# Performance work log

Hardware: AMD Instinct MI355X
Metric: run time of the kernel (lower is better)

Reference implementation:

```python
import jax, jax.numpy as jnp
import numpy as np

N, R, H, OUT = 512, 16, 16, 1
EPSILON = 1e-6
CUTOFF = 5.0  # ExpNormalSmearing cutoff_upper (cutoff_lower = 0)


def exp_normal_smearing(dist):
    # dist: (N, N, 1) -> (N, N, R); TorchMD-Net style ExpNormalSmearing
    start = jnp.exp(-CUTOFF)
    means = jnp.linspace(start, 1.0, R, dtype=dist.dtype)
    beta = (2.0 / R * (1.0 - start)) ** -2
    cutoff = 0.5 * (jnp.cos(dist * jnp.pi / CUTOFF) + 1.0) * (dist < CUTOFF)
    return cutoff * jnp.exp(-beta * (jnp.exp(-dist) - means) ** 2)


def setup_inputs() -> dict:
    key = jax.random.key(0)
    ks = jax.random.split(key, 9)
    s_in = 1.0 / np.sqrt(H * H)
    s_h = 1.0 / np.sqrt(H)
    return {
        "x": jax.random.normal(ks[0], (N, 3), jnp.float32) * 1.5,
        "W": jax.random.normal(ks[1], (2, N, R, H), jnp.float32) * 0.1,
        "W1": jax.random.normal(ks[2], (H, H * H), jnp.float32) * s_in,
        "b1": jax.random.normal(ks[3], (H,), jnp.float32) * 0.01,
        "W2": jax.random.normal(ks[4], (4 * R * H, H), jnp.float32) * s_h,
        "W3": jax.random.normal(ks[5], (H, H * H), jnp.float32) * s_in,
        "b3": jax.random.normal(ks[6], (H,), jnp.float32) * 0.01,
        "W4": jax.random.normal(ks[7], (OUT, H), jnp.float32) * s_h,
        "b4": jax.random.normal(ks[8], (OUT,), jnp.float32) * 0.01,
    }


def reference(x, W, W1, b1, W2, W3, b3, W4, b4):
    K, Q = W[0], W[1]                               # (N, R, H) each
    diff = x[:, None, :] - x[None, :, :]            # (N, N, 3)
    nsq = jnp.sum(diff * diff, axis=-1, keepdims=True) + EPSILON
    norm = jnp.sqrt(nsq)                            # (N, N, 1)
    diff = diff / nsq                               # note: divided by squared norm (faithful)
    sm = exp_normal_smearing(norm)                  # (N, N, R)
    basis = sm[..., None] * diff[..., None, :]      # (N, N, R, 3)

    bk = jnp.einsum('ijrb,jrc->icb', basis, K)      # (N, H, 3)
    bq = jnp.einsum('ijrb,jrc->icb', basis, Q)
    att = jnp.einsum('ihb,igb->ihg', bk, bq).reshape(N, H * H)
    att = jax.nn.silu(att @ W1.T + b1) @ W2.T       # (N, 4*R*H), second Linear bias-free

    left, right = att[:, : 2 * R * H], att[:, 2 * R * H:]
    pair = left[:, None, :] + right[None, :, :]     # (N, N, 2*R*H)
    K2 = pair[..., : R * H].reshape(N, N, R, H)
    Q2 = pair[..., R * H:].reshape(N, N, R, H)

    bk = jnp.einsum('ijrb,ijrc->icb', basis, K2)    # (N, H, 3)
    bq = jnp.einsum('ijrb,ijrc->icb', basis, Q2)
    att = jnp.einsum('ihb,igb->ihg', bk, bq).reshape(N, H * H)
    return jax.nn.silu(att @ W3.T + b3) @ W4.T + b4  # (N, OUT)
```

## Files before the change

kernel.cpp:

```cpp
#include <hip/hip_runtime.h>
#include <math.h>

#define NN 512

#define START 0.006737946999085467f
#define STEP  ((1.0f - START) * (1.0f/15.0f))
#define SB    (0.125f * (1.0f - START))
#define BETA  (1.0f/(SB*SB))
#define LOG2E 1.4426950408889634f
#define NB    (-(BETA)*LOG2E)


__global__ __launch_bounds__(256) void k0(const float* __restrict__ W,
                                          float* __restrict__ Wt)
{
    __shared__ float ldsb[256];
    const int row = blockIdx.x;
    ldsb[threadIdx.x] = W[(size_t)row*256 + threadIdx.x];
    __syncthreads();
    const int c = threadIdx.x >> 4, r = threadIdx.x & 15;
    Wt[(size_t)row*256 + threadIdx.x] = ldsb[r*16 + c];
}

__device__ __forceinline__ void dot16(
    float4 g0, float4 g1, float4 g2, float4 g3,
    float4 ka, float4 kb, float4 kc, float4 kd,
    float4 qa, float4 qb, float4 qc, float4 qd,
    float& tk, float& tq)
{
    tk = g0.x*ka.x; tq = g0.x*qa.x;
    tk = fmaf(g0.y,ka.y,tk); tq = fmaf(g0.y,qa.y,tq);
    tk = fmaf(g0.z,ka.z,tk); tq = fmaf(g0.z,qa.z,tq);
    tk = fmaf(g0.w,ka.w,tk); tq = fmaf(g0.w,qa.w,tq);
    tk = fmaf(g1.x,kb.x,tk); tq = fmaf(g1.x,qb.x,tq);
    tk = fmaf(g1.y,kb.y,tk); tq = fmaf(g1.y,qb.y,tq);
    tk = fmaf(g1.z,kb.z,tk); tq = fmaf(g1.z,qb.z,tq);
    tk = fmaf(g1.w,kb.w,tk); tq = fmaf(g1.w,qb.w,tq);
    tk = fmaf(g2.x,kc.x,tk); tq = fmaf(g2.x,qc.x,tq);
    tk = fmaf(g2.y,kc.y,tk); tq = fmaf(g2.y,qc.y,tq);
    tk = fmaf(g2.z,kc.z,tk); tq = fmaf(g2.z,qc.z,tq);
    tk = fmaf(g2.w,kc.w,tk); tq = fmaf(g2.w,qc.w,tq);
    tk = fmaf(g3.x,kd.x,tk); tq = fmaf(g3.x,qd.x,tq);
    tk = fmaf(g3.y,kd.y,tk); tq = fmaf(g3.y,qd.y,tq);
    tk = fmaf(g3.z,kd.z,tk); tq = fmaf(g3.z,qd.z,tq);
    tk = fmaf(g3.w,kd.w,tk); tq = fmaf(g3.w,qd.w,tq);
}

__global__ __launch_bounds__(256) void k1a(const float* __restrict__ x,
                                           const float* __restrict__ Wt,
                                           float* __restrict__ part1)
{
    const int ib = blockIdx.x & 127, jc = blockIdx.x >> 7;
    const int i0 = ib * 4;
    const int tid = threadIdx.x;
    const int c = tid & 15, js = tid >> 4;
    const int lane = tid & 63, wv = tid >> 6;

    __shared__ float  lG[4][64][16];
    __shared__ float4 lP[4][64];
    __shared__ float  s_part[4][16][26];

    {
        const int pi = tid >> 6, pj = tid & 63;
        const int jg = jc*64 + pj;
        const float xi0 = x[(i0+pi)*3+0], xi1 = x[(i0+pi)*3+1], xi2 = x[(i0+pi)*3+2];
        float d0 = xi0 - x[jg*3+0];
        float d1 = xi1 - x[jg*3+1];
        float d2 = xi2 - x[jg*3+2];
        float nsq = fmaf(d0,d0, fmaf(d1,d1, fmaf(d2,d2, 1e-6f)));
        float rs  = __builtin_amdgcn_rsqf(nsq);
        float nrm = nsq * rs;
        float inv = rs * rs;
        float cutv = 0.f;
        if (nrm < 5.0f) cutv = 0.5f*(__cosf(nrm*0.6283185307179586f)+1.0f);
        float en = exp2f(-LOG2E * nrm);
        lP[pi][pj] = make_float4(d0*inv, d1*inv, d2*inv, 0.f);
        float4* dst = reinterpret_cast<float4*>(&lG[pi][pj][0]);
        #pragma unroll
        for (int rq = 0; rq < 4; ++rq) {
            float t0 = en - (START + STEP*(float)(4*rq+0));
            float t1 = en - (START + STEP*(float)(4*rq+1));
            float t2 = en - (START + STEP*(float)(4*rq+2));
            float t3 = en - (START + STEP*(float)(4*rq+3));
            dst[rq] = make_float4(cutv*exp2f(NB*t0*t0), cutv*exp2f(NB*t1*t1),
                                  cutv*exp2f(NB*t2*t2), cutv*exp2f(NB*t3*t3));
        }
    }
    __syncthreads();

    float acc[24];
    #pragma unroll
    for (int v = 0; v < 24; ++v) acc[v] = 0.f;

    const float4* Kp = reinterpret_cast<const float4*>(Wt + (size_t)(jc*64 + js)*256 + c*16);
    const float4* Qp = reinterpret_cast<const float4*>(Wt + (size_t)NN*256 + (size_t)(jc*64 + js)*256 + c*16);
    float4 ka = Kp[0], kb = Kp[1], kc = Kp[2], kd = Kp[3];
    float4 qa = Qp[0], qb = Qp[1], qc = Qp[2], qd = Qp[3];

    #pragma unroll 1
    for (int t = 0; t < 4; ++t) {
        float4 nka, nkb, nkc, nkd, nqa, nqb, nqc, nqd;
        if (t < 3) {
            const float4* Kn = Kp + (size_t)(t+1)*16*64;
            const float4* Qn = Qp + (size_t)(t+1)*16*64;
            nka = Kn[0]; nkb = Kn[1]; nkc = Kn[2]; nkd = Kn[3];
            nqa = Qn[0]; nqb = Qn[1]; nqc = Qn[2]; nqd = Qn[3];
        }
        const int jl = js + 16*t;

        #pragma unroll
        for (int i = 0; i < 4; ++i) {
            const float4* gp = reinterpret_cast<const float4*>(&lG[i][jl][0]);
            float tk, tq;
            dot16(gp[0], gp[1], gp[2], gp[3], ka,kb,kc,kd, qa,qb,qc,qd, tk, tq);
            float4 dd = lP[i][jl];
            acc[i*6+0] = fmaf(tk, dd.x, acc[i*6+0]);
            acc[i*6+1] = fmaf(tk, dd.y, acc[i*6+1]);
            acc[i*6+2] = fmaf(tk, dd.z, acc[i*6+2]);
            acc[i*6+3] = fmaf(tq, dd.x, acc[i*6+3]);
            acc[i*6+4] = fmaf(tq, dd.y, acc[i*6+4]);
            acc[i*6+5] = fmaf(tq, dd.z, acc[i*6+5]);
        }
        if (t < 3) { ka=nka; kb=nkb; kc=nkc; kd=nkd; qa=nqa; qb=nqb; qc=nqc; qd=nqd; }
    }

    #pragma unroll
    for (int v = 0; v < 24; ++v) {
        float t = acc[v];
        t += __shfl_xor(t, 16);
        t += __shfl_xor(t, 32);
        if (lane < 16) s_part[wv][c][v] = t;
    }
    __syncthreads();

    for (int v = tid; v < 384; v += 256) {
        int i = v / 96, o = v - i*96;
        int kq = o / 48, rem = o - kq*48;
        int b = rem >> 4, c2 = rem & 15;
        int f = i*6 + kq*3 + b;
        float sum = s_part[0][c2][f] + s_part[1][c2][f]
                  + s_part[2][c2][f] + s_part[3][c2][f];
        part1[(i0+i)*768 + jc*96 + o] = sum;
    }
}

__global__ __launch_bounds__(256) void k1b(const float* __restrict__ part1,
                                           const float* __restrict__ W1,
                                           const float* __restrict__ b1,
                                           const float* __restrict__ W2,
                                           float* __restrict__ att2t)
{
    const int i = blockIdx.x;
    const int tid = threadIdx.x;
    __shared__ float s_bkq[96];
    __shared__ float s_att[256];
    __shared__ float s_z[16][16];
    __shared__ float s_a1[16];

    if (tid < 96) {
        const float* p = part1 + i*768 + tid;
        float s = 0.f;
        #pragma unroll
        for (int k = 0; k < 8; ++k) s += p[k*96];
        s_bkq[tid] = s;
    }
    __syncthreads();

    {
        int h = tid >> 4, g = tid & 15;
        s_att[tid] = s_bkq[     h]*s_bkq[48+     g]
                   + s_bkq[16 + h]*s_bkq[48+16 + g]
                   + s_bkq[32 + h]*s_bkq[48+32 + g];
    }
    __syncthreads();

    {
        int h = tid & 15, seg = tid >> 4;
        const float* w1 = W1 + h*256 + seg*16;
        const float* a  = s_att + seg*16;
        float p = 0.f;
        #pragma unroll
        for (int k = 0; k < 16; ++k) p = fmaf(a[k], w1[k], p);
        s_z[seg][h] = p;
    }
    __syncthreads();

    if (tid < 16) {
        float z = b1[tid];
        #pragma unroll
        for (int seg = 0; seg < 16; ++seg) z += s_z[seg][tid];
        s_a1[tid] = z / (1.0f + __expf(-z));
    }
    __syncthreads();

    float a1[16];
    #pragma unroll
    for (int cc = 0; cc < 16; ++cc) a1[cc] = s_a1[cc];
    #pragma unroll
    for (int p = 0; p < 4; ++p) {
        int o = tid + p*256;
        const float4* w2 = reinterpret_cast<const float4*>(W2 + o*16);
        float4 wa = w2[0], wb = w2[1], wc = w2[2], wd = w2[3];
        float accv = wa.x*a1[0] + wa.y*a1[1] + wa.z*a1[2] + wa.w*a1[3]
                   + wb.x*a1[4] + wb.y*a1[5] + wb.z*a1[6] + wb.w*a1[7]
                   + wc.x*a1[8] + wc.y*a1[9] + wc.z*a1[10]+ wc.w*a1[11]
                   + wd.x*a1[12]+ wd.y*a1[13]+ wd.z*a1[14]+ wd.w*a1[15];
        att2t[i*1024 + ((o>>8)*256) + ((o&15)*16) + ((o>>4)&15)] = accv;
    }
}

__global__ __launch_bounds__(256) void k2a(const float* __restrict__ x,
                                           const float* __restrict__ att2t,
                                           float* __restrict__ part2)
{
    const int ib = blockIdx.x & 127, jc = blockIdx.x >> 7;
    const int i0 = ib * 4;
    const int tid = threadIdx.x;
    const int c = tid & 15, js = tid >> 4;
    const int lane = tid & 63, wv = tid >> 6;

    __shared__ float  lG[4][64][16];
    __shared__ float4 lP[4][64];
    __shared__ float  s_part[4][16][38];

    {
        const int pi = tid >> 6, pj = tid & 63;
        const int jg = jc*64 + pj;
        const float xi0 = x[(i0+pi)*3+0], xi1 = x[(i0+pi)*3+1], xi2 = x[(i0+pi)*3+2];
        float d0 = xi0 - x[jg*3+0];
        float d1 = xi1 - x[jg*3+1];
        float d2 = xi2 - x[jg*3+2];
        float nsq = fmaf(d0,d0, fmaf(d1,d1, fmaf(d2,d2, 1e-6f)));
        float rs  = __builtin_amdgcn_rsqf(nsq);
        float nrm = nsq * rs;
        float inv = rs * rs;
        float cutv = 0.f;
        if (nrm < 5.0f) cutv = 0.5f*(__cosf(nrm*0.6283185307179586f)+1.0f);
        float en = exp2f(-LOG2E * nrm);
        lP[pi][pj] = make_float4(d0*inv, d1*inv, d2*inv, 0.f);
        float4* dst = reinterpret_cast<float4*>(&lG[pi][pj][0]);
        #pragma unroll
        for (int rq = 0; rq < 4; ++rq) {
            float t0 = en - (START + STEP*(float)(4*rq+0));
            float t1 = en - (START + STEP*(float)(4*rq+1));
            float t2 = en - (START + STEP*(float)(4*rq+2));
            float t3 = en - (START + STEP*(float)(4*rq+3));
            dst[rq] = make_float4(cutv*exp2f(NB*t0*t0), cutv*exp2f(NB*t1*t1),
                                  cutv*exp2f(NB*t2*t2), cutv*exp2f(NB*t3*t3));
        }
    }
    __syncthreads();

    float acc[36];
    #pragma unroll
    for (int v = 0; v < 36; ++v) acc[v] = 0.f;

    const float4* Kp = reinterpret_cast<const float4*>(att2t + (size_t)(jc*64 + js)*1024 + 512 + c*16);
    const float4* Qp = reinterpret_cast<const float4*>(att2t + (size_t)(jc*64 + js)*1024 + 768 + c*16);
    float4 ka = Kp[0], kb = Kp[1], kc = Kp[2], kd = Kp[3];
    float4 qa = Qp[0], qb = Qp[1], qc = Qp[2], qd = Qp[3];

    #pragma unroll 1
    for (int t = 0; t < 4; ++t) {
        float4 nka, nkb, nkc, nkd, nqa, nqb, nqc, nqd;
        if (t < 3) {
            const float4* Kn = Kp + (size_t)(t+1)*16*256;
            const float4* Qn = Qp + (size_t)(t+1)*16*256;
            nka = Kn[0]; nkb = Kn[1]; nkc = Kn[2]; nkd = Kn[3];
            nqa = Qn[0]; nqb = Qn[1]; nqc = Qn[2]; nqd = Qn[3];
        }
        const int jl = js + 16*t;

        #pragma unroll
        for (int i = 0; i < 4; ++i) {
            const float4* gp = reinterpret_cast<const float4*>(&lG[i][jl][0]);
            float tk, tq;
            dot16(gp[0], gp[1], gp[2], gp[3], ka,kb,kc,kd, qa,qb,qc,qd, tk, tq);
            float4 dd = lP[i][jl];
            acc[i*6+0] = fmaf(tk, dd.x, acc[i*6+0]);
            acc[i*6+1] = fmaf(tk, dd.y, acc[i*6+1]);
            acc[i*6+2] = fmaf(tk, dd.z, acc[i*6+2]);
            acc[i*6+3] = fmaf(tq, dd.x, acc[i*6+3]);
            acc[i*6+4] = fmaf(tq, dd.y, acc[i*6+4]);
            acc[i*6+5] = fmaf(tq, dd.z, acc[i*6+5]);
            float gc = lG[i][jl][c];
            acc[24+i*3+0] = fmaf(gc, dd.x, acc[24+i*3+0]);
            acc[24+i*3+1] = fmaf(gc, dd.y, acc[24+i*3+1]);
            acc[24+i*3+2] = fmaf(gc, dd.z, acc[24+i*3+2]);
        }
        if (t < 3) { ka=nka; kb=nkb; kc=nkc; kd=nkd; qa=nqa; qb=nqb; qc=nqc; qd=nqd; }
    }

    #pragma unroll
    for (int v = 0; v < 36; ++v) {
        float t = acc[v];
        t += __shfl_xor(t, 16);
        t += __shfl_xor(t, 32);
        if (lane < 16) s_part[wv][c][v] = t;
    }
    __syncthreads();

    for (int v = tid; v < 576; v += 256) {
        int i = v / 144, o = v - i*144;
        int c2, f;
        if (o < 96) {
            int kq = o / 48, rem = o - kq*48;
            int b = rem >> 4; c2 = rem & 15;
            f = i*6 + kq*3 + b;
        } else {
            int oS = o - 96;
            int r = oS / 3, b = oS - r*3;
            c2 = r;
            f = 24 + i*3 + b;
        }
        float sum = s_part[0][c2][f] + s_part[1][c2][f]
                  + s_part[2][c2][f] + s_part[3][c2][f];
        part2[(i0+i)*1152 + jc*144 + o] = sum;
    }
}

__global__ __launch_bounds__(256) void k2b(const float* __restrict__ att2t,
                                           const float* __restrict__ part2,
                                           const float* __restrict__ W3,
                                           const float* __restrict__ b3,
                                           const float* __restrict__ W4,
                                           const float* __restrict__ b4,
                                           float* __restrict__ out)
{
    const int i = blockIdx.x;
    const int tid = threadIdx.x;
    __shared__ float s_red[144];
    __shared__ float s_att[256];
    __shared__ float s_z[16][16];
    __shared__ float s_a1[16];

    if (tid < 144) {
        const float* p = part2 + i*1152 + tid;
        float s = 0.f;
        #pragma unroll
        for (int k = 0; k < 8; ++k) s += p[k*144];
        s_red[tid] = s;
    }
    __syncthreads();

    if (tid < 96) {
        int kq = tid / 48, rem = tid - kq*48;
        int b = rem >> 4, cc = rem & 15;
        const float4* lrow = reinterpret_cast<const float4*>(att2t + i*1024 + kq*256 + cc*16);
        float4 A = lrow[0], B = lrow[1], C = lrow[2], D = lrow[3];
        float add = 0.f;
        add = fmaf(A.x, s_red[96+ 0*3+b], add);
        add = fmaf(A.y, s_red[96+ 1*3+b], add);
        add = fmaf(A.z, s_red[96+ 2*3+b], add);
        add = fmaf(A.w, s_red[96+ 3*3+b], add);
        add = fmaf(B.x, s_red[96+ 4*3+b], add);
        add = fmaf(B.y, s_red[96+ 5*3+b], add);
        add = fmaf(B.z, s_red[96+ 6*3+b], add);
        add = fmaf(B.w, s_red[96+ 7*3+b], add);
        add = fmaf(C.x, s_red[96+ 8*3+b], add);
        add = fmaf(C.y, s_red[96+ 9*3+b], add);
        add = fmaf(C.z, s_red[96+10*3+b], add);
        add = fmaf(C.w, s_red[96+11*3+b], add);
        add = fmaf(D.x, s_red[96+12*3+b], add);
        add = fmaf(D.y, s_red[96+13*3+b], add);
        add = fmaf(D.z, s_red[96+14*3+b], add);
        add = fmaf(D.w, s_red[96+15*3+b], add);
        s_red[tid] += add;
    }
    __syncthreads();

    {
        int h = tid >> 4, g = tid & 15;
        s_att[tid] = s_red[     h]*s_red[48+     g]
                   + s_red[16 + h]*s_red[48+16 + g]
                   + s_red[32 + h]*s_red[48+32 + g];
    }
    __syncthreads();

    {
        int h = tid & 15, seg = tid >> 4;
        const float* w3 = W3 + h*256 + seg*16;
        const float* a  = s_att + seg*16;
        float p = 0.f;
        #pragma unroll
        for (int k = 0; k < 16; ++k) p = fmaf(a[k], w3[k], p);
        s_z[seg][h] = p;
    }
    __syncthreads();

    if (tid < 16) {
        float z = b3[tid];
        #pragma unroll
        for (int seg = 0; seg < 16; ++seg) z += s_z[seg][tid];
        s_a1[tid] = z / (1.0f + __expf(-z));
    }
    __syncthreads();

    if (tid == 0) {
        float accv = b4[0];
        #pragma unroll
        for (int cc = 0; cc < 16; ++cc) accv = fmaf(s_a1[cc], W4[cc], accv);
        out[i] = accv;
    }
}

extern "C" void kernel_launch(void* const* d_in, const int* in_sizes, int n_in,
                              void* d_out, int out_size, void* d_ws, size_t ws_size,
                              hipStream_t stream) {
    (void)in_sizes; (void)n_in; (void)out_size; (void)ws_size;
    const float* x  = (const float*)d_in[0];
    const float* W  = (const float*)d_in[1];
    const float* W1 = (const float*)d_in[2];
    const float* b1 = (const float*)d_in[3];
    const float* W2 = (const float*)d_in[4];
    const float* W3 = (const float*)d_in[5];
    const float* b3 = (const float*)d_in[6];
    const float* W4 = (const float*)d_in[7];
    const float* b4 = (const float*)d_in[8];

    float* att2t = (float*)d_ws;
    float* part1 = att2t + 512*1024;
    float* part2 = part1 + 512*768;
    float* Wt    = part2 + 512*1152;
    float* out   = (float*)d_out;

    k0 <<<1024, 256, 0, stream>>>(W, Wt);
    k1a<<<1024, 256, 0, stream>>>(x, Wt, part1);
    k1b<<< 512, 256, 0, stream>>>(part1, W1, b1, W2, att2t);
    k2a<<<1024, 256, 0, stream>>>(x, att2t, part2);
    k2b<<< 512, 256, 0, stream>>>(att2t, part2, W3, b3, W4, b4, out);
}
```

Before: 120.9 us.

## Fuse reduction/MLP stages into partial kernels via last-block atomic tickets

Merges k1b into k1a and k2b into k2a. Each block publishes its partial sums with relaxed atomic stores and bumps a per-row-group ticket, and the eighth block to arrive does the cross-chunk reduction and the MLP epilogue for its 4 rows. This removes two kernel launches and their inter-kernel gaps, and tickets are reset in k0. It also drops the register double-buffered prefetch of K/Q in the j-loop, which could expose load latency. The ordering relies only on relaxed atomics with no explicit fences, which carries a memory-visibility risk.

```diff
diff --git a/kernel.cpp b/kernel.cpp
--- a/kernel.cpp
+++ b/kernel.cpp
@@ -11,12 +11,17 @@
 #define NB    (-(BETA)*LOG2E)
 
 
+#define ATOMIC_ST(p, v) __hip_atomic_store((p), (v), __ATOMIC_RELAXED, __HIP_MEMORY_SCOPE_AGENT)
+#define ATOMIC_LD(p)    __hip_atomic_load((p), __ATOMIC_RELAXED, __HIP_MEMORY_SCOPE_AGENT)
+
 __global__ __launch_bounds__(256) void k0(const float* __restrict__ W,
-                                          float* __restrict__ Wt)
+                                          float* __restrict__ Wt,
+                                          unsigned* __restrict__ tick)
 {
     __shared__ float ldsb[256];
     const int row = blockIdx.x;
     ldsb[threadIdx.x] = W[(size_t)row*256 + threadIdx.x];
+    if (blockIdx.x == 0) tick[threadIdx.x] = 0;
     __syncthreads();
     const int c = threadIdx.x >> 4, r = threadIdx.x & 15;
     Wt[(size_t)row*256 + threadIdx.x] = ldsb[r*16 + c];
@@ -46,9 +51,14 @@
     tk = fmaf(g3.w,kd.w,tk); tq = fmaf(g3.w,qd.w,tq);
 }
 
-__global__ __launch_bounds__(256) void k1a(const float* __restrict__ x,
-                                           const float* __restrict__ Wt,
-                                           float* __restrict__ part1)
+__global__ __launch_bounds__(256) void k1(const float* __restrict__ x,
+                                          const float* __restrict__ Wt,
+                                          float* __restrict__ part1,
+                                          const float* __restrict__ W1,
+                                          const float* __restrict__ b1,
+                                          const float* __restrict__ W2,
+                                          float* __restrict__ att2t,
+                                          unsigned* __restrict__ tick)
 {
     const int ib = blockIdx.x & 127, jc = blockIdx.x >> 7;
     const int i0 = ib * 4;
@@ -56,9 +66,15 @@
     const int c = tid & 15, js = tid >> 4;
     const int lane = tid & 63, wv = tid >> 6;
 
-    __shared__ float  lG[4][64][16];
+    __shared__ __align__(16) float  lG[4][64][16];
     __shared__ float4 lP[4][64];
-    __shared__ float  s_part[4][16][26];
+    __shared__ __align__(16) char u_sc[8192];
+    float (*s_part)[16][26] = reinterpret_cast<float(*)[16][26]>(u_sc);
+    float (*s_attf)[256]    = reinterpret_cast<float(*)[256]>(u_sc);
+    float (*s_zf)[16][16]   = reinterpret_cast<float(*)[16][16]>(u_sc + 4096);
+    __shared__ float s_bkq[4][96];
+    __shared__ float s_a1[4][16];
+    __shared__ int   s_flag;
 
     {
         const int pi = tid >> 6, pj = tid & 63;
@@ -92,21 +108,14 @@
     #pragma unroll
     for (int v = 0; v < 24; ++v) acc[v] = 0.f;
 
-    const float4* Kp = reinterpret_cast<const float4*>(Wt + (size_t)(jc*64 + js)*256 + c*16);
-    const float4* Qp = reinterpret_cast<const float4*>(Wt + (size_t)NN*256 + (size_t)(jc*64 + js)*256 + c*16);
-    float4 ka = Kp[0], kb = Kp[1], kc = Kp[2], kd = Kp[3];
-    float4 qa = Qp[0], qb = Qp[1], qc = Qp[2], qd = Qp[3];
-
     #pragma unroll 1
     for (int t = 0; t < 4; ++t) {
-        float4 nka, nkb, nkc, nkd, nqa, nqb, nqc, nqd;
-        if (t < 3) {
-            const float4* Kn = Kp + (size_t)(t+1)*16*64;
-            const float4* Qn = Qp + (size_t)(t+1)*16*64;
-            nka = Kn[0]; nkb = Kn[1]; nkc = Kn[2]; nkd = Kn[3];
-            nqa = Qn[0]; nqb = Qn[1]; nqc = Qn[2]; nqd = Qn[3];
-        }
         const int jl = js + 16*t;
+        const int jg = jc*64 + jl;
+        const float4* Kp = reinterpret_cast<const float4*>(Wt + (size_t)jg*256 + c*16);
+        const float4* Qp = reinterpret_cast<const float4*>(Wt + (size_t)NN*256 + (size_t)jg*256 + c*16);
+        float4 ka = Kp[0], kb = Kp[1], kc = Kp[2], kd = Kp[3];
+        float4 qa = Qp[0], qb = Qp[1], qc = Qp[2], qd = Qp[3];
 
         #pragma unroll
         for (int i = 0; i < 4; ++i) {
@@ -121,7 +130,6 @@
             acc[i*6+4] = fmaf(tq, dd.y, acc[i*6+4]);
             acc[i*6+5] = fmaf(tq, dd.z, acc[i*6+5]);
         }
-        if (t < 3) { ka=nka; kb=nkb; kc=nkc; kd=nkd; qa=nqa; qb=nqb; qc=nqc; qd=nqd; }
     }
 
     #pragma unroll
@@ -140,78 +148,88 @@
         int f = i*6 + kq*3 + b;
         float sum = s_part[0][c2][f] + s_part[1][c2][f]
                   + s_part[2][c2][f] + s_part[3][c2][f];
-        part1[(i0+i)*768 + jc*96 + o] = sum;
-    }
-}
-
-__global__ __launch_bounds__(256) void k1b(const float* __restrict__ part1,
-                                           const float* __restrict__ W1,
-                                           const float* __restrict__ b1,
-                                           const float* __restrict__ W2,
-                                           float* __restrict__ att2t)
-{
-    const int i = blockIdx.x;
-    const int tid = threadIdx.x;
-    __shared__ float s_bkq[96];
-    __shared__ float s_att[256];
-    __shared__ float s_z[16][16];
-    __shared__ float s_a1[16];
-
-    if (tid < 96) {
-        const float* p = part1 + i*768 + tid;
+        ATOMIC_ST(&part1[(i0+i)*768 + jc*96 + o], sum);
+    }
+    __syncthreads();
+
+    if (tid == 0) {
+        unsigned old = __hip_atomic_fetch_add(&tick[ib], 1u,
+                        __ATOMIC_RELAXED, __HIP_MEMORY_SCOPE_AGENT);
+        s_flag = (old == 7u);
+    }
+    __syncthreads();
+    if (!s_flag) return;
+
+    for (int v = tid; v < 384; v += 256) {
+        int ii = v / 96, o = v - ii*96;
+        const float* p = part1 + (i0+ii)*768 + o;
         float s = 0.f;
         #pragma unroll
-        for (int k = 0; k < 8; ++k) s += p[k*96];
-        s_bkq[tid] = s;
-    }
-    __syncthreads();
-
-    {
-        int h = tid >> 4, g = tid & 15;
-        s_att[tid] = s_bkq[     h]*s_bkq[48+     g]
-                   + s_bkq[16 + h]*s_bkq[48+16 + g]
-                   + s_bkq[32 + h]*s_bkq[48+32 + g];
+        for (int k = 0; k < 8; ++k) s += ATOMIC_LD(p + k*96);
+        s_bkq[ii][o] = s;
+    }
+    __syncthreads();
+
+    for (int v = tid; v < 1024; v += 256) {
+        int ii = v >> 8, t2 = v & 255;
+        int h = t2 >> 4, g = t2 & 15;
+        s_attf[ii][t2] = s_bkq[ii][     h]*s_bkq[ii][48+     g]
+                       + s_bkq[ii][16 + h]*s_bkq[ii][48+16 + g]
+                       + s_bkq[ii][32 + h]*s_bkq[ii][48+32 + g];
     }
     __syncthreads();
 
     {
         int h = tid & 15, seg = tid >> 4;
         const float* w1 = W1 + h*256 + seg*16;
-        const float* a  = s_att + seg*16;
-        float p = 0.f;
-        #pragma unroll
-        for (int k = 0; k < 16; ++k) p = fmaf(a[k], w1[k], p);
-        s_z[seg][h] = p;
-    }
-    __syncthreads();
-
-    if (tid < 16) {
-        float z = b1[tid];
-        #pragma unroll
-        for (int seg = 0; seg < 16; ++seg) z += s_z[seg][tid];
-        s_a1[tid] = z / (1.0f + __expf(-z));
-    }
-    __syncthreads();
-
-    float a1[16];
-    #pragma unroll
-    for (int cc = 0; cc < 16; ++cc) a1[cc] = s_a1[cc];
-    #pragma unroll
-    for (int p = 0; p < 4; ++p) {
-        int o = tid + p*256;
-        const float4* w2 = reinterpret_cast<const float4*>(W2 + o*16);
-        float4 wa = w2[0], wb = w2[1], wc = w2[2], wd = w2[3];
-        float accv = wa.x*a1[0] + wa.y*a1[1] + wa.z*a1[2] + wa.w*a1[3]
-                   + wb.x*a1[4] + wb.y*a1[5] + wb.z*a1[6] + wb.w*a1[7]
-                   + wc.x*a1[8] + wc.y*a1[9] + wc.z*a1[10]+ wc.w*a1[11]
-                   + wd.x*a1[12]+ wd.y*a1[13]+ wd.z*a1[14]+ wd.w*a1[15];
-        att2t[i*1024 + ((o>>8)*256) + ((o&15)*16) + ((o>>4)&15)] = accv;
+        #pragma unroll
+        for (int ii = 0; ii < 4; ++ii) {
+            const float* a = &s_attf[ii][seg*16];
+            float p = 0.f;
+            #pragma unroll
+            for (int k = 0; k < 16; ++k) p = fmaf(a[k], w1[k], p);
+            s_zf[ii][seg][h] = p;
+        }
+    }
+    __syncthreads();
+
+    if (tid < 64) {
+        int ii = tid >> 4, h = tid & 15;
+        float z = b1[h];
+        #pragma unroll
+        for (int seg = 0; seg < 16; ++seg) z += s_zf[ii][seg][h];
+        s_a1[ii][h] = z / (1.0f + __expf(-z));
+    }
+    __syncthreads();
+
+    #pragma unroll 1
+    for (int ii = 0; ii < 4; ++ii) {
+        float a1[16];
+        #pragma unroll
+        for (int cc = 0; cc < 16; ++cc) a1[cc] = s_a1[ii][cc];
+        #pragma unroll
+        for (int p = 0; p < 4; ++p) {
+            int o = tid + p*256;
+            const float4* w2 = reinterpret_cast<const float4*>(W2 + o*16);
+            float4 wa = w2[0], wb = w2[1], wc = w2[2], wd = w2[3];
+            float accv = wa.x*a1[0] + wa.y*a1[1] + wa.z*a1[2] + wa.w*a1[3]
+                       + wb.x*a1[4] + wb.y*a1[5] + wb.z*a1[6] + wb.w*a1[7]
+                       + wc.x*a1[8] + wc.y*a1[9] + wc.z*a1[10]+ wc.w*a1[11]
+                       + wd.x*a1[12]+ wd.y*a1[13]+ wd.z*a1[14]+ wd.w*a1[15];
+            att2t[(i0+ii)*1024 + ((o>>8)*256) + ((o&15)*16) + ((o>>4)&15)] = accv;
+        }
     }
 }
 
-__global__ __launch_bounds__(256) void k2a(const float* __restrict__ x,
-                                           const float* __restrict__ att2t,
-                                           float* __restrict__ part2)
+__global__ __launch_bounds__(256) void k2(const float* __restrict__ x,
+                                          const float* __restrict__ att2t,
+                                          float* __restrict__ part2,
+                                          const float* __restrict__ W3,
+                                          const float* __restrict__ b3,
+                                          const float* __restrict__ W4,
+                                          const float* __restrict__ b4,
+                                          float* __restrict__ out,
+                                          unsigned* __restrict__ tick)
 {
     const int ib = blockIdx.x & 127, jc = blockIdx.x >> 7;
     const int i0 = ib * 4;
@@ -219,9 +237,15 @@
     const int c = tid & 15, js = tid >> 4;
     const int lane = tid & 63, wv = tid >> 6;
 
-    __shared__ float  lG[4][64][16];
+    __shared__ __align__(16) float  lG[4][64][16];
     __shared__ float4 lP[4][64];
-    __shared__ float  s_part[4][16][38];
+    __shared__ __align__(16) char u_sc[9728];
+    float (*s_part)[16][38] = reinterpret_cast<float(*)[16][38]>(u_sc);
+    float (*s_attf)[256]    = reinterpret_cast<float(*)[256]>(u_sc);
+    float (*s_zf)[16][16]   = reinterpret_cast<float(*)[16][16]>(u_sc + 4096);
+    __shared__ float s_red[4][144];
+    __shared__ float s_a1[4][16];
+    __shared__ int   s_flag;
 
     {
         const int pi = tid >> 6, pj = tid & 63;
@@ -255,21 +279,14 @@
     #pragma unroll
     for (int v = 0; v < 36; ++v) acc[v] = 0.f;
 
-    const float4* Kp = reinterpret_cast<const float4*>(att2t + (size_t)(jc*64 + js)*1024 + 512 + c*16);
-    const float4* Qp = reinterpret_cast<const float4*>(att2t + (size_t)(jc*64 + js)*1024 + 768 + c*16);
-    float4 ka = Kp[0], kb = Kp[1], kc = Kp[2], kd = Kp[3];
-    float4 qa = Qp[0], qb = Qp[1], qc = Qp[2], qd = Qp[3];
-
     #pragma unroll 1
     for (int t = 0; t < 4; ++t) {
-        float4 nka, nkb, nkc, nkd, nqa, nqb, nqc, nqd;
-        if (t < 3) {
-            const float4* Kn = Kp + (size_t)(t+1)*16*256;
-            const float4* Qn = Qp + (size_t)(t+1)*16*256;
-            nka = Kn[0]; nkb = Kn[1]; nkc = Kn[2]; nkd = Kn[3];
-            nqa = Qn[0]; nqb = Qn[1]; nqc = Qn[2]; nqd = Qn[3];
-        }
         const int jl = js + 16*t;
+        const int jg = jc*64 + jl;
+        const float4* Kp = reinterpret_cast<const float4*>(att2t + (size_t)jg*1024 + 512 + c*16);
+        const float4* Qp = reinterpret_cast<const float4*>(att2t + (size_t)jg*1024 + 768 + c*16);
+        float4 ka = Kp[0], kb = Kp[1], kc = Kp[2], kd = Kp[3];
+        float4 qa = Qp[0], qb = Qp[1], qc = Qp[2], qd = Qp[3];
 
         #pragma unroll
         for (int i = 0; i < 4; ++i) {
@@ -288,7 +305,6 @@
             acc[24+i*3+1] = fmaf(gc, dd.y, acc[24+i*3+1]);
             acc[24+i*3+2] = fmaf(gc, dd.z, acc[24+i*3+2]);
         }
-        if (t < 3) { ka=nka; kb=nkb; kc=nkc; kd=nkd; qa=nqa; qb=nqb; qc=nqc; qd=nqd; }
     }
 
     #pragma unroll
@@ -315,92 +331,93 @@
         }
         float sum = s_part[0][c2][f] + s_part[1][c2][f]
                   + s_part[2][c2][f] + s_part[3][c2][f];
-        part2[(i0+i)*1152 + jc*144 + o] = sum;
-    }
-}
-
-__global__ __launch_bounds__(256) void k2b(const float* __restrict__ att2t,
-                                           const float* __restrict__ part2,
-                                           const float* __restrict__ W3,
-                                           const float* __restrict__ b3,
-                                           const float* __restrict__ W4,
-                                           const float* __restrict__ b4,
-                                           float* __restrict__ out)
-{
-    const int i = blockIdx.x;
-    const int tid = threadIdx.x;
-    __shared__ float s_red[144];
-    __shared__ float s_att[256];
-    __shared__ float s_z[16][16];
-    __shared__ float s_a1[16];
-
-    if (tid < 144) {
-        const float* p = part2 + i*1152 + tid;
+        ATOMIC_ST(&part2[(i0+i)*1152 + jc*144 + o], sum);
+    }
+    __syncthreads();
+
+    if (tid == 0) {
+        unsigned old = __hip_atomic_fetch_add(&tick[128 + ib], 1u,
+                        __ATOMIC_RELAXED, __HIP_MEMORY_SCOPE_AGENT);
+        s_flag = (old == 7u);
+    }
+    __syncthreads();
+    if (!s_flag) return;
+
+    for (int v = tid; v < 576; v += 256) {
+        int ii = v / 144, o = v - ii*144;
+        const float* p = part2 + (i0+ii)*1152 + o;
         float s = 0.f;
         #pragma unroll
-        for (int k = 0; k < 8; ++k) s += p[k*144];
-        s_red[tid] = s;
-    }
-    __syncthreads();
-
-    if (tid < 96) {
-        int kq = tid / 48, rem = tid - kq*48;
+        for (int k = 0; k < 8; ++k) s += ATOMIC_LD(p + k*144);
+        s_red[ii][o] = s;
+    }
+    __syncthreads();
+
+    for (int v = tid; v < 384; v += 256) {
+        int ii = v / 96, t96 = v - ii*96;
+        int kq = t96 / 48, rem = t96 - kq*48;
         int b = rem >> 4, cc = rem & 15;
-        const float4* lrow = reinterpret_cast<const float4*>(att2t + i*1024 + kq*256 + cc*16);
+        const float4* lrow = reinterpret_cast<const float4*>(att2t + (i0+ii)*1024 + kq*256 + cc*16);
         float4 A = lrow[0], B = lrow[1], C = lrow[2], D = lrow[3];
         float add = 0.f;
-        add = fmaf(A.x, s_red[96+ 0*3+b], add);
-        add = fmaf(A.y, s_red[96+ 1*3+b], add);
-        add = fmaf(A.z, s_red[96+ 2*3+b], add);
-        add = fmaf(A.w, s_red[96+ 3*3+b], add);
-        add = fmaf(B.x, s_red[96+ 4*3+b], add);
-        add = fmaf(B.y, s_red[96+ 5*3+b], add);
-        add = fmaf(B.z, s_red[96+ 6*3+b], add);
-        add = fmaf(B.w, s_red[96+ 7*3+b], add);
-        add = fmaf(C.x, s_red[96+ 8*3+b], add);
-        add = fmaf(C.y, s_red[96+ 9*3+b], add);
-        add = fmaf(C.z, s_red[96+10*3+b], add);
-        add = fmaf(C.w, s_red[96+11*3+b], add);
-        add = fmaf(D.x, s_red[96+12*3+b], add);
-        add = fmaf(D.y, s_red[96+13*3+b], add);
-        add = fmaf(D.z, s_red[96+14*3+b], add);
-        add = fmaf(D.w, s_red[96+15*3+b], add);
-        s_red[tid] += add;
-    }
-    __syncthreads();
-
-    {
-        int h = tid >> 4, g = tid & 15;
-        s_att[tid] = s_red[     h]*s_red[48+     g]
-                   + s_red[16 + h]*s_red[48+16 + g]
-                   + s_red[32 + h]*s_red[48+32 + g];
+        add = fmaf(A.x, s_red[ii][96+ 0*3+b], add);
+        add = fmaf(A.y, s_red[ii][96+ 1*3+b], add);
+        add = fmaf(A.z, s_red[ii][96+ 2*3+b], add);
+        add = fmaf(A.w, s_red[ii][96+ 3*3+b], add);
+        add = fmaf(B.x, s_red[ii][96+ 4*3+b], add);
+        add = fmaf(B.y, s_red[ii][96+ 5*3+b], add);
+        add = fmaf(B.z, s_red[ii][96+ 6*3+b], add);
+        add = fmaf(B.w, s_red[ii][96+ 7*3+b], add);
+        add = fmaf(C.x, s_red[ii][96+ 8*3+b], add);
+        add = fmaf(C.y, s_red[ii][96+ 9*3+b], add);
+        add = fmaf(C.z, s_red[ii][96+10*3+b], add);
+        add = fmaf(C.w, s_red[ii][96+11*3+b], add);
+        add = fmaf(D.x, s_red[ii][96+12*3+b], add);
+        add = fmaf(D.y, s_red[ii][96+13*3+b], add);
+        add = fmaf(D.z, s_red[ii][96+14*3+b], add);
+        add = fmaf(D.w, s_red[ii][96+15*3+b], add);
+        s_red[ii][t96] += add;
+    }
+    __syncthreads();
+
+    for (int v = tid; v < 1024; v += 256) {
+        int ii = v >> 8, t2 = v & 255;
+        int h = t2 >> 4, g = t2 & 15;
+        s_attf[ii][t2] = s_red[ii][     h]*s_red[ii][48+     g]
+                       + s_red[ii][16 + h]*s_red[ii][48+16 + g]
+                       + s_red[ii][32 + h]*s_red[ii][48+32 + g];
     }
     __syncthreads();
 
     {
         int h = tid & 15, seg = tid >> 4;
         const float* w3 = W3 + h*256 + seg*16;
-        const float* a  = s_att + seg*16;
-        float p = 0.f;
-        #pragma unroll
-        for (int k = 0; k < 16; ++k) p = fmaf(a[k], w3[k], p);
-        s_z[seg][h] = p;
-    }
-    __syncthreads();
-
-    if (tid < 16) {
-        float z = b3[tid];
-        #pragma unroll
-        for (int seg = 0; seg < 16; ++seg) z += s_z[seg][tid];
-        s_a1[tid] = z / (1.0f + __expf(-z));
-    }
-    __syncthreads();
-
-    if (tid == 0) {
+        #pragma unroll
+        for (int ii = 0; ii < 4; ++ii) {
+            const float* a = &s_attf[ii][seg*16];
+            float p = 0.f;
+            #pragma unroll
+            for (int k = 0; k < 16; ++k) p = fmaf(a[k], w3[k], p);
+            s_zf[ii][seg][h] = p;
+        }
+    }
+    __syncthreads();
+
+    if (tid < 64) {
+        int ii = tid >> 4, h = tid & 15;
+        float z = b3[h];
+        #pragma unroll
+        for (int seg = 0; seg < 16; ++seg) z += s_zf[ii][seg][h];
+        s_a1[ii][h] = z / (1.0f + __expf(-z));
+    }
+    __syncthreads();
+
+    if (tid < 4) {
+        int ii = tid;
         float accv = b4[0];
         #pragma unroll
-        for (int cc = 0; cc < 16; ++cc) accv = fmaf(s_a1[cc], W4[cc], accv);
-        out[i] = accv;
+        for (int cc = 0; cc < 16; ++cc) accv = fmaf(s_a1[ii][cc], W4[cc], accv);
+        out[i0+ii] = accv;
     }
 }
 
@@ -422,11 +439,10 @@
     float* part1 = att2t + 512*1024;
     float* part2 = part1 + 512*768;
     float* Wt    = part2 + 512*1152;
+    unsigned* tick = (unsigned*)(Wt + 2*512*256);
     float* out   = (float*)d_out;
 
-    k0 <<<1024, 256, 0, stream>>>(W, Wt);
-    k1a<<<1024, 256, 0, stream>>>(x, Wt, part1);
-    k1b<<< 512, 256, 0, stream>>>(part1, W1, b1, W2, att2t);
-    k2a<<<1024, 256, 0, stream>>>(x, att2t, part2);
-    k2b<<< 512, 256, 0, stream>>>(att2t, part2, W3, b3, W4, b4, out);
+    k0<<<1024, 256, 0, stream>>>(W, Wt, tick);
+    k1<<<1024, 256, 0, stream>>>(x, Wt, part1, W1, b1, W2, att2t, tick);
+    k2<<<1024, 256, 0, stream>>>(x, att2t, part2, W3, b3, W4, b4, out, tick);
 }
```

Measured after the change: 123.3 us. About the same (+2.0%).
